# Kernel optimization log

Measured on AMD Instinct MI355X. Metric: run time of the kernel, lower is better.

Reference implementation:

```python
import jax, jax.numpy as jnp
import numpy as np

EPS = 1e-5

def _ln(x):
    # LayerNorm without affine (elementwise_affine=False when adaLN=True)
    m = jnp.mean(x, axis=-1, keepdims=True)
    v = jnp.mean((x - m) ** 2, axis=-1, keepdims=True)
    return (x - m) / jnp.sqrt(v + EPS)

def _ln_affine(x, g, b):
    return _ln(x) * g + b

def setup_inputs() -> dict:
    key = jax.random.key(0)
    B, L, D, H, P = 2, 1024, 1024, 16, 64
    FF = 4 * D
    ks = jax.random.split(key, 16)
    s = 0.02
    inp = {
        'x': jax.random.normal(ks[0], (B, L, D), jnp.float32),
        'z': jax.random.normal(ks[1], (B, L, L, P), jnp.float32),
        'trans': jax.random.normal(ks[2], (B, L, 3), jnp.float32),
        'mask': jnp.ones((B, L), jnp.bool_),
        'x_cond': jax.random.normal(ks[3], (B, L, D), jnp.float32),
        # adaLN modulation: SiLU -> Linear(D, 6D). (Randomly init'd; the torch
        # code zero-inits it, which would zero the whole block output.)
        'ada_W': jax.random.normal(ks[4], (D, 6 * D), jnp.float32) * s,
        'ada_b': jnp.zeros((6 * D,), jnp.float32),
        # attention projections (torch Linear weights stored as [in, out])
        'Wq': jax.random.normal(ks[5], (D, D), jnp.float32) * s,
        'bq': jnp.zeros((D,), jnp.float32),
        'Wk': jax.random.normal(ks[6], (D, D), jnp.float32) * s,
        'bk': jnp.zeros((D,), jnp.float32),
        'Wv': jax.random.normal(ks[7], (D, D), jnp.float32) * s,
        'bv': jnp.zeros((D,), jnp.float32),
        'Wo': jax.random.normal(ks[8], (D, D), jnp.float32) * s,
        'bo': jnp.zeros((D,), jnp.float32),
        # FeedForward: LayerNorm(D) (affine) -> Linear(D,FF) -> ReLU -> Linear(FF,D)
        'ln_g': jnp.ones((D,), jnp.float32),
        'ln_b': jnp.zeros((D,), jnp.float32),
        'W1': jax.random.normal(ks[9], (D, FF), jnp.float32) * s,
        'b1': jnp.zeros((FF,), jnp.float32),
        'W2': jax.random.normal(ks[10], (FF, D), jnp.float32) * s,
        'b2': jnp.zeros((D,), jnp.float32),
    }
    return inp

def _block(x, z, trans, mask, x_cond, ada_W, ada_b, Wq, bq, Wk, bk, Wv, bv,
           Wo, bo, ln_g, ln_b, W1, b1, W2, b2):
    B, L, D = x.shape
    H = 16
    dh = D // H
    # adaLN modulation from conditioning signal
    c = jax.nn.silu(x_cond) @ ada_W + ada_b
    (shift_mha, scale_mha, gate_mha,
     shift_mlp, scale_mlp, gate_mlp) = jnp.split(c, 6, axis=-1)
    # --- attention branch: norm -> modulate -> MHA -> gate -> residual ---
    h = _ln(x) * (1.0 + scale_mha) + shift_mha
    q = (h @ Wq + bq).reshape(B, L, H, dh)
    k = (h @ Wk + bk).reshape(B, L, H, dh)
    v = (h @ Wv + bv).reshape(B, L, H, dh)
    scores = jnp.einsum('blhd,bmhd->bhlm', q, k) / jnp.sqrt(jnp.float32(dh))
    neg = jnp.finfo(scores.dtype).min
    scores = jnp.where(mask[:, None, None, :], scores, neg)
    attn = jax.nn.softmax(scores, axis=-1)
    o = jnp.einsum('bhlm,bmhd->blhd', attn, v).reshape(B, L, D)
    mha_out = o @ Wo + bo
    x = x + mha_out * gate_mha
    # --- FFN branch: norm -> modulate -> FF(LN, Lin, ReLU, Lin) -> gate ---
    h = _ln(x) * (1.0 + scale_mlp) + shift_mlp
    h = _ln_affine(h, ln_g, ln_b)
    h = jax.nn.relu(h @ W1 + b1)
    ff_out = h @ W2 + b2
    x = x + ff_out * gate_mlp
    # pair_updates=False, frame_update=False: z and trans pass through
    return x, z, trans

def reference(x, z, trans, mask, x_cond, ada_W, ada_b, Wq, bq, Wk, bk, Wv, bv,
              Wo, bo, ln_g, ln_b, W1, b1, W2, b2):
    return _block(x, z, trans, mask, x_cond, ada_W, ada_b, Wq, bq, Wk, bk,
                  Wv, bv, Wo, bo, ln_g, ln_b, W1, b1, W2, b2)
```

## Files before the change

kernel.cpp:

```cpp
#include <hip/hip_runtime.h>
#include <hip/hip_bf16.h>


typedef __attribute__((ext_vector_type(8))) __bf16 bf16x8;
typedef __attribute__((ext_vector_type(4))) float f32x4;
typedef __attribute__((ext_vector_type(8))) unsigned short ushortx8;

#define DEVI static __device__ __forceinline__

DEVI unsigned short f2bf(float f) {
    __hip_bfloat16 h = __float2bfloat16(f);
    return __builtin_bit_cast(unsigned short, h);
}

DEVI void gload16(const void* g, void* l) {
    __builtin_amdgcn_global_load_lds(
        (const __attribute__((address_space(1))) void*)g,
        (__attribute__((address_space(3))) void*)l, 16, 0, 0);
}

DEVI void side_copy(const float4* __restrict__ src, float4* __restrict__ dst,
                    long long off, long long len, long long cb, long long ncb) {
    const long long nthr = ncb * 256;
    for (long long i = cb * 256 + threadIdx.x; i < len; i += nthr)
        dst[off + i] = src[off + i];
}

__global__ __launch_bounds__(256) void transpose_cast(
        const float* __restrict__ in, unsigned short* __restrict__ out,
        int K, int N) {
    __shared__ float tile[32][33];
    const int n0 = blockIdx.x * 32, k0 = blockIdx.y * 32;
    const int tx = threadIdx.x, ty = threadIdx.y;
#pragma unroll
    for (int i = 0; i < 4; ++i)
        tile[ty + 8 * i][tx] = in[(size_t)(k0 + ty + 8 * i) * N + n0 + tx];
    __syncthreads();
#pragma unroll
    for (int i = 0; i < 4; ++i)
        out[(size_t)(n0 + ty + 8 * i) * K + k0 + tx] = f2bf(tile[tx][ty + 8 * i]);
}

__global__ __launch_bounds__(256) void silu_cast(
        const float* __restrict__ x, unsigned short* __restrict__ o) {
    const int i = blockIdx.x * 256 + threadIdx.x;
    float4 v = ((const float4*)x)[i];
    ushort4 r;
    r.x = f2bf(v.x / (1.f + __expf(-v.x)));
    r.y = f2bf(v.y / (1.f + __expf(-v.y)));
    r.z = f2bf(v.z / (1.f + __expf(-v.z)));
    r.w = f2bf(v.w / (1.f + __expf(-v.w)));
    ((ushort4*)o)[i] = r;
}

__global__ void concat3(const float* __restrict__ a, const float* __restrict__ b,
                        const float* __restrict__ c, float* __restrict__ o, int D) {
    const int i = blockIdx.x * 256 + threadIdx.x;
    if (i < D) o[i] = a[i];
    else if (i < 2 * D) o[i] = b[i - D];
    else if (i < 3 * D) o[i] = c[i - 2 * D];
}

template <int MODE, int MT>
__global__ __launch_bounds__(256) void gemm_bt(
        const unsigned short* __restrict__ A, const unsigned short* __restrict__ Bt,
        const float* __restrict__ bias,
        float* __restrict__ outf, unsigned short* __restrict__ outb,
        const float* __restrict__ res, const float* __restrict__ gate, int gstride,
        int M, int N, int K,
        unsigned short* __restrict__ vt, int twoD, int H, int Lr,
        const float4* __restrict__ cp_src, float4* __restrict__ cp_dst,
        long long cp_off, long long cp_len, int gy) {
    if ((int)blockIdx.y >= gy) {
        const long long cb = (long long)(blockIdx.y - gy) * gridDim.x + blockIdx.x;
        const long long ncb = (long long)(gridDim.y - gy) * gridDim.x;
        side_copy(cp_src, cp_dst, cp_off, cp_len, cb, ncb);
        return;
    }
    __shared__ __align__(16) unsigned short lA[MT * 32 * 32];
    __shared__ __align__(16) unsigned short lB[128 * 32];
    const int tid = threadIdx.x;
    const int wave = tid >> 6, lane = tid & 63;
    const int fr = lane & 15, fg = lane >> 4;
    const int wr = wave >> 1, wc = wave & 1;
    const int m0 = blockIdx.y * (MT * 32), n0 = blockIdx.x * 128;

    f32x4 acc[MT][4];
#pragma unroll
    for (int i = 0; i < MT; ++i)
#pragma unroll
        for (int j = 0; j < 4; ++j) acc[i][j] = (f32x4){0.f, 0.f, 0.f, 0.f};

    for (int k0 = 0; k0 < K; k0 += 32) {
#pragma unroll
        for (int ch = 0; ch < 2; ++ch) {
            const int p = ch * 4096 + wave * 1024 + lane * 16;
            const int row = p >> 6, kb = p & 63;
            if (ch < MT / 2)
                gload16((const char*)A + ((size_t)(m0 + row) * K + k0) * 2 + kb, (char*)lA + p);
            gload16((const char*)Bt + ((size_t)(n0 + row) * K + k0) * 2 + kb, (char*)lB + p);
        }
        __syncthreads();
        bf16x8 af[MT], bfm[4];
#pragma unroll
        for (int t = 0; t < MT; ++t)
            af[t] = *(const bf16x8*)((const char*)lA + ((wr * (MT * 16) + t * 16 + fr) * 32 + fg * 8) * 2);
#pragma unroll
        for (int t = 0; t < 4; ++t)
            bfm[t] = *(const bf16x8*)((const char*)lB + ((wc * 64 + t * 16 + fr) * 32 + fg * 8) * 2);
#pragma unroll
        for (int mt = 0; mt < MT; ++mt)
#pragma unroll
            for (int nt = 0; nt < 4; ++nt)
                acc[mt][nt] = __builtin_amdgcn_mfma_f32_16x16x32_bf16(
                        af[mt], bfm[nt], acc[mt][nt], 0, 0, 0);
        __syncthreads();
    }
#pragma unroll
    for (int mt = 0; mt < MT; ++mt)
#pragma unroll
        for (int nt = 0; nt < 4; ++nt) {
            const int gcol = n0 + wc * 64 + nt * 16 + fr;
            const float bb = bias[gcol];
#pragma unroll
            for (int j = 0; j < 4; ++j) {
                const int grow = m0 + wr * (MT * 16) + mt * 16 + fg * 4 + j;
                const size_t idx = (size_t)grow * N + gcol;
                const float v = acc[mt][nt][j] + bb;
                if constexpr (MODE == 0) outf[idx] = v;
                else if constexpr (MODE == 1) outb[idx] = f2bf(v);
                else if constexpr (MODE == 2) outf[idx] = res[idx] + v * gate[(size_t)grow * gstride + gcol];
                else if constexpr (MODE == 3) outb[idx] = f2bf(fmaxf(v, 0.f));
                else {
                    const unsigned short bv16 = f2bf(v);
                    outb[idx] = bv16;
                    if (gcol >= twoD) {
                        const int d = gcol - twoD, hh = d >> 6, dd = d & 63;
                        const int bb2 = grow >= Lr ? 1 : 0, l = grow - bb2 * Lr;
                        vt[((size_t)(bb2 * H + hh) * 64 + dd) * Lr + l] = bv16;
                    }
                }
            }
        }
}

__global__ __launch_bounds__(256) void ln_mod(
        const float* __restrict__ x, const float* __restrict__ c,
        unsigned short* __restrict__ h, int D, int cs) {
    const int row = blockIdx.x, tid = threadIdx.x;
    const int lane = tid & 63, wave = tid >> 6;
    const float4 xv = ((const float4*)(x + (size_t)row * D))[tid];
    float s = xv.x + xv.y + xv.z + xv.w;
    float ss = xv.x * xv.x + xv.y * xv.y + xv.z * xv.z + xv.w * xv.w;
#pragma unroll
    for (int o = 1; o < 64; o <<= 1) { s += __shfl_xor(s, o); ss += __shfl_xor(ss, o); }
    __shared__ float red[8];
    if (lane == 0) { red[wave] = s; red[4 + wave] = ss; }
    __syncthreads();
    s = red[0] + red[1] + red[2] + red[3];
    ss = red[4] + red[5] + red[6] + red[7];
    const float mean = s / D;
    const float rstd = rsqrtf(ss / D - mean * mean + 1e-5f);
    const float* crow = c + (size_t)row * cs;
    const float4 sh = ((const float4*)(crow))[tid];
    const float4 sc = ((const float4*)(crow + D))[tid];
    ushort4 r;
    r.x = f2bf((xv.x - mean) * rstd * (1.f + sc.x) + sh.x);
    r.y = f2bf((xv.y - mean) * rstd * (1.f + sc.y) + sh.y);
    r.z = f2bf((xv.z - mean) * rstd * (1.f + sc.z) + sh.z);
    r.w = f2bf((xv.w - mean) * rstd * (1.f + sc.w) + sh.w);
    ((ushort4*)(h + (size_t)row * D))[tid] = r;
}

__global__ __launch_bounds__(256) void ln2_mod(
        const float* __restrict__ x2, const float* __restrict__ c,
        const float* __restrict__ g, const float* __restrict__ bb,
        unsigned short* __restrict__ h, int D, int cs) {
    const int row = blockIdx.x, tid = threadIdx.x;
    const int lane = tid & 63, wave = tid >> 6;
    const float4 xv = ((const float4*)(x2 + (size_t)row * D))[tid];
    float s = xv.x + xv.y + xv.z + xv.w;
    float ss = xv.x * xv.x + xv.y * xv.y + xv.z * xv.z + xv.w * xv.w;
#pragma unroll
    for (int o = 1; o < 64; o <<= 1) { s += __shfl_xor(s, o); ss += __shfl_xor(ss, o); }
    __shared__ float red[16];
    if (lane == 0) { red[wave] = s; red[4 + wave] = ss; }
    __syncthreads();
    s = red[0] + red[1] + red[2] + red[3];
    ss = red[4] + red[5] + red[6] + red[7];
    const float mean = s / D;
    const float rstd = rsqrtf(ss / D - mean * mean + 1e-5f);
    const float* crow = c + (size_t)row * cs;
    const float4 sh = ((const float4*)(crow + 3 * D))[tid];
    const float4 sc = ((const float4*)(crow + 4 * D))[tid];
    float t[4];
    t[0] = (xv.x - mean) * rstd * (1.f + sc.x) + sh.x;
    t[1] = (xv.y - mean) * rstd * (1.f + sc.y) + sh.y;
    t[2] = (xv.z - mean) * rstd * (1.f + sc.z) + sh.z;
    t[3] = (xv.w - mean) * rstd * (1.f + sc.w) + sh.w;
    float s2 = t[0] + t[1] + t[2] + t[3];
    float ss2 = t[0] * t[0] + t[1] * t[1] + t[2] * t[2] + t[3] * t[3];
#pragma unroll
    for (int o = 1; o < 64; o <<= 1) { s2 += __shfl_xor(s2, o); ss2 += __shfl_xor(ss2, o); }
    if (lane == 0) { red[8 + wave] = s2; red[12 + wave] = ss2; }
    __syncthreads();
    s2 = red[8] + red[9] + red[10] + red[11];
    ss2 = red[12] + red[13] + red[14] + red[15];
    const float mean2 = s2 / D;
    const float rstd2 = rsqrtf(ss2 / D - mean2 * mean2 + 1e-5f);
    const float4 gv = ((const float4*)g)[tid];
    const float4 bv = ((const float4*)bb)[tid];
    ushort4 r;
    r.x = f2bf((t[0] - mean2) * rstd2 * gv.x + bv.x);
    r.y = f2bf((t[1] - mean2) * rstd2 * gv.y + bv.y);
    r.z = f2bf((t[2] - mean2) * rstd2 * gv.z + bv.z);
    r.w = f2bf((t[3] - mean2) * rstd2 * gv.w + bv.w);
    ((ushort4*)(h + (size_t)row * D))[tid] = r;
}

__global__ __launch_bounds__(256) void attn_fwd(
        const unsigned short* __restrict__ qkv, const unsigned short* __restrict__ vt,
        unsigned short* __restrict__ o,
        int L, int D, int B,
        const float4* __restrict__ cp_src, float4* __restrict__ cp_dst,
        long long cp_off, long long cp_len) {
    if ((int)blockIdx.z >= B) {
        const long long cb = (long long)(blockIdx.z - B) * gridDim.x * gridDim.y
                           + (long long)blockIdx.y * gridDim.x + blockIdx.x;
        const long long ncb = (long long)(gridDim.z - B) * gridDim.x * gridDim.y;
        side_copy(cp_src, cp_dst, cp_off, cp_len, cb, ncb);
        return;
    }
    const int q0 = blockIdx.x * 64, hh = blockIdx.y, b = blockIdx.z;
    const int H = gridDim.y;
    const int tid = threadIdx.x, wave = tid >> 6, lane = tid & 63;
    const int fr = lane & 15, fg = lane >> 4;
    const size_t rs = 3 * (size_t)D;
    const unsigned short* vtb = vt + (size_t)(b * H + hh) * 64 * L;
    __shared__ __align__(16) unsigned short lK[64 * 72];
    __shared__ __align__(16) unsigned short lVT[64 * 72];
    __shared__ __align__(16) unsigned short lP[4 * 16 * 72];

    bf16x8 aq[2];
    {
        const size_t qr = (size_t)(b * L + q0 + wave * 16 + fr);
#pragma unroll
        for (int kk = 0; kk < 2; ++kk)
            aq[kk] = *(const bf16x8*)(qkv + qr * rs + hh * 64 + kk * 32 + fg * 8);
    }
    f32x4 oacc[4];
#pragma unroll
    for (int i = 0; i < 4; ++i) oacc[i] = (f32x4){0.f, 0.f, 0.f, 0.f};
    float m_run[4] = {-1e30f, -1e30f, -1e30f, -1e30f};
    float l_run[4] = {0.f, 0.f, 0.f, 0.f};

    for (int n0 = 0; n0 < L; n0 += 64) {
        __syncthreads();
#pragma unroll
        for (int it = 0; it < 2; ++it) {
            const int idx = it * 256 + tid, r = idx >> 3, cc = idx & 7;
            const unsigned short* src = qkv + (size_t)(b * L + n0 + r) * rs + D + hh * 64 + cc * 8;
            *(ushortx8*)(&lK[r * 72 + cc * 8]) = *(const ushortx8*)src;
        }
#pragma unroll
        for (int it = 0; it < 2; ++it) {
            const int idx = it * 256 + tid, r = idx >> 3, cc = idx & 7;
            *(ushortx8*)(&lVT[r * 72 + cc * 8]) =
                *(const ushortx8*)(vtb + (size_t)r * L + n0 + cc * 8);
        }
        __syncthreads();
        f32x4 sfr[4];
#pragma unroll
        for (int nt = 0; nt < 4; ++nt) {
            const bf16x8 bk0 = *(const bf16x8*)((const char*)lK + ((nt * 16 + fr) * 72 + fg * 8) * 2);
            const bf16x8 bk1 = *(const bf16x8*)((const char*)lK + ((nt * 16 + fr) * 72 + 32 + fg * 8) * 2);
            f32x4 t = (f32x4){0.f, 0.f, 0.f, 0.f};
            t = __builtin_amdgcn_mfma_f32_16x16x32_bf16(aq[0], bk0, t, 0, 0, 0);
            t = __builtin_amdgcn_mfma_f32_16x16x32_bf16(aq[1], bk1, t, 0, 0, 0);
#pragma unroll
            for (int j = 0; j < 4; ++j) t[j] *= 0.125f;
            sfr[nt] = t;
        }
        float tm[4], prs[4], alpha[4];
#pragma unroll
        for (int j = 0; j < 4; ++j) {
            float v = fmaxf(fmaxf(sfr[0][j], sfr[1][j]), fmaxf(sfr[2][j], sfr[3][j]));
#pragma unroll
            for (int off = 1; off < 16; off <<= 1) v = fmaxf(v, __shfl_xor(v, off));
            tm[j] = v;
        }
#pragma unroll
        for (int j = 0; j < 4; ++j) {
            const float mn = fmaxf(m_run[j], tm[j]);
            alpha[j] = __expf(m_run[j] - mn);
            m_run[j] = mn;
            prs[j] = 0.f;
        }
#pragma unroll
        for (int nt = 0; nt < 4; ++nt)
#pragma unroll
            for (int j = 0; j < 4; ++j) {
                const float p = __expf(sfr[nt][j] - m_run[j]);
                sfr[nt][j] = p;
                prs[j] += p;
            }
#pragma unroll
        for (int j = 0; j < 4; ++j) {
#pragma unroll
            for (int off = 1; off < 16; off <<= 1) prs[j] += __shfl_xor(prs[j], off);
            l_run[j] = l_run[j] * alpha[j] + prs[j];
        }
#pragma unroll
        for (int dt = 0; dt < 4; ++dt)
#pragma unroll
            for (int j = 0; j < 4; ++j) oacc[dt][j] *= alpha[j];
        unsigned short* pw = &lP[wave * 16 * 72];
#pragma unroll
        for (int nt = 0; nt < 4; ++nt)
#pragma unroll
            for (int j = 0; j < 4; ++j)
                pw[(fg * 4 + j) * 72 + nt * 16 + fr] = f2bf(sfr[nt][j]);
        const bf16x8 ap0 = *(const bf16x8*)((const char*)pw + (fr * 72 + fg * 8) * 2);
        const bf16x8 ap1 = *(const bf16x8*)((const char*)pw + (fr * 72 + 32 + fg * 8) * 2);
#pragma unroll
        for (int dt = 0; dt < 4; ++dt) {
            const bf16x8 bv0 = *(const bf16x8*)((const char*)lVT + ((dt * 16 + fr) * 72 + fg * 8) * 2);
            const bf16x8 bv1 = *(const bf16x8*)((const char*)lVT + ((dt * 16 + fr) * 72 + 32 + fg * 8) * 2);
            oacc[dt] = __builtin_amdgcn_mfma_f32_16x16x32_bf16(ap0, bv0, oacc[dt], 0, 0, 0);
            oacc[dt] = __builtin_amdgcn_mfma_f32_16x16x32_bf16(ap1, bv1, oacc[dt], 0, 0, 0);
        }
    }
    float inv[4];
#pragma unroll
    for (int j = 0; j < 4; ++j) inv[j] = 1.f / l_run[j];
#pragma unroll
    for (int dt = 0; dt < 4; ++dt)
#pragma unroll
        for (int j = 0; j < 4; ++j) {
            const int orow = b * L + q0 + wave * 16 + fg * 4 + j;
            o[(size_t)orow * D + hh * 64 + dt * 16 + fr] = f2bf(oacc[dt][j] * inv[j]);
        }
}

extern "C" void kernel_launch(void* const* d_in, const int* in_sizes, int n_in,
                              void* d_out, int out_size, void* d_ws, size_t ws_size,
                              hipStream_t stream) {
    (void)n_in; (void)out_size;
    const float* x      = (const float*)d_in[0];
    const float* z      = (const float*)d_in[1];
    const float* trans  = (const float*)d_in[2];
    const float* x_cond = (const float*)d_in[4];
    const float* ada_W  = (const float*)d_in[5];
    const float* ada_b  = (const float*)d_in[6];
    const float* Wq = (const float*)d_in[7];  const float* bq = (const float*)d_in[8];
    const float* Wk = (const float*)d_in[9];  const float* bk = (const float*)d_in[10];
    const float* Wv = (const float*)d_in[11]; const float* bv = (const float*)d_in[12];
    const float* Wo = (const float*)d_in[13]; const float* bo = (const float*)d_in[14];
    const float* ln_g = (const float*)d_in[15]; const float* ln_b = (const float*)d_in[16];
    const float* W1 = (const float*)d_in[17]; const float* b1 = (const float*)d_in[18];
    const float* W2 = (const float*)d_in[19]; const float* b2 = (const float*)d_in[20];

    const int D  = in_sizes[6] / 6;
    const int FF = in_sizes[18];
    const int M  = in_sizes[0] / D;
    const int B  = 2, L = M / B, H = 16;
    const size_t zN = (size_t)in_sizes[1], tN = (size_t)in_sizes[2];

    float* out_x = (float*)d_out;
    float* out_z = out_x + (size_t)M * D;
    float* out_t = out_z + zN;

    size_t off = 0;
    auto alloc = [&](size_t bytes) { size_t o = off; off += (bytes + 255) & ~(size_t)255; return o; };
    const size_t o_adaWt = alloc((size_t)6 * D * D * 2);
    const size_t o_Wqkvt = alloc((size_t)3 * D * D * 2);
    const size_t o_Wot   = alloc((size_t)D * D * 2);
    const size_t o_W1t   = alloc((size_t)FF * D * 2);
    const size_t o_W2t   = alloc((size_t)D * FF * 2);
    const size_t o_bqkv  = alloc((size_t)3 * D * 4);
    const size_t o_xcb   = alloc((size_t)M * D * 2);
    const size_t o_c     = alloc((size_t)M * 6 * D * 4);
    const size_t o_hb    = alloc((size_t)M * D * 2);
    const size_t o_qkv   = alloc((size_t)M * 3 * D * 2);
    const size_t o_vt    = alloc((size_t)M * D * 2);
    const size_t o_ob    = alloc((size_t)M * D * 2);
    const size_t o_x2    = alloc((size_t)M * D * 4);
    const size_t o_h2b   = alloc((size_t)M * D * 2);
    const size_t o_f1    = alloc((size_t)M * FF * 2);
    const size_t need = off;
    const bool have_ws = (ws_size >= need);
    char* base = have_ws ? (char*)d_ws : (char*)out_z;

    unsigned short* adaWt = (unsigned short*)(base + o_adaWt);
    unsigned short* Wqkvt = (unsigned short*)(base + o_Wqkvt);
    unsigned short* Wot   = (unsigned short*)(base + o_Wot);
    unsigned short* W1t   = (unsigned short*)(base + o_W1t);
    unsigned short* W2t   = (unsigned short*)(base + o_W2t);
    float*          bqkv  = (float*)(base + o_bqkv);
    unsigned short* xcb   = (unsigned short*)(base + o_xcb);
    float*          cbuf  = (float*)(base + o_c);
    unsigned short* hb    = (unsigned short*)(base + o_hb);
    unsigned short* qkvb  = (unsigned short*)(base + o_qkv);
    unsigned short* vtb   = (unsigned short*)(base + o_vt);
    unsigned short* ob    = (unsigned short*)(base + o_ob);
    float*          x2    = (float*)(base + o_x2);
    unsigned short* h2b   = (unsigned short*)(base + o_h2b);
    unsigned short* f1b   = (unsigned short*)(base + o_f1);

    const float4* zs = (const float4*)z;
    float4* zd = (float4*)out_z;
    const long long zN4 = (long long)(zN / 4);
    long long c0 = 0, c1 = 0, c2 = 0, c3 = 0, c4 = 0, c5 = 0;
    int e0 = 0, e1 = 0, e2 = 0, e3 = 0, e4 = 0, e5 = 0;
    if (have_ws) {
        c0 = zN4 / 4;  c1 = zN4 / 8;  c2 = zN4 / 4;  c3 = zN4 / 16;  c4 = zN4 / 4;
        c5 = zN4 - (c0 + c1 + c2 + c3 + c4);
        e0 = 8; e1 = 16; e2 = 1; e3 = 16; e4 = 12; e5 = 24;
    }
    const long long s0 = 0, s1 = s0 + c0, s2 = s1 + c1, s3 = s2 + c2, s4 = s3 + c3, s5 = s4 + c4;

    const dim3 tb(32, 8);
    transpose_cast<<<dim3(6 * D / 32, D / 32), tb, 0, stream>>>(ada_W, adaWt, D, 6 * D);
    transpose_cast<<<dim3(D / 32, D / 32), tb, 0, stream>>>(Wq, Wqkvt, D, D);
    transpose_cast<<<dim3(D / 32, D / 32), tb, 0, stream>>>(Wk, Wqkvt + (size_t)D * D, D, D);
    transpose_cast<<<dim3(D / 32, D / 32), tb, 0, stream>>>(Wv, Wqkvt + (size_t)2 * D * D, D, D);
    transpose_cast<<<dim3(D / 32, D / 32), tb, 0, stream>>>(Wo, Wot, D, D);
    transpose_cast<<<dim3(FF / 32, D / 32), tb, 0, stream>>>(W1, W1t, D, FF);
    transpose_cast<<<dim3(D / 32, FF / 32), tb, 0, stream>>>(W2, W2t, FF, D);
    concat3<<<(3 * D + 255) / 256, 256, 0, stream>>>(bq, bk, bv, bqkv, D);
    silu_cast<<<M * D / 1024, 256, 0, stream>>>(x_cond, xcb);

    const int gy128 = M / 128, gy64 = M / 64;
    gemm_bt<0, 4><<<dim3(6 * D / 128, gy128 + e0), 256, 0, stream>>>(
            xcb, adaWt, ada_b, cbuf, nullptr, nullptr, nullptr, 0, M, 6 * D, D,
            nullptr, 0, 0, 0, zs, zd, s0, c0, gy128);
    ln_mod<<<M, 256, 0, stream>>>(x, cbuf, hb, D, 6 * D);
    gemm_bt<4, 4><<<dim3(3 * D / 128, gy128 + e1), 256, 0, stream>>>(
            hb, Wqkvt, bqkv, nullptr, qkvb, nullptr, nullptr, 0, M, 3 * D, D,
            vtb, 2 * D, H, L, zs, zd, s1, c1, gy128);
    attn_fwd<<<dim3(L / 64, H, B + e2), 256, 0, stream>>>(qkvb, vtb, ob, L, D, B,
            zs, zd, s2, c2);
    gemm_bt<2, 2><<<dim3(D / 128, gy64 + e3), 256, 0, stream>>>(
            ob, Wot, bo, x2, nullptr, x, cbuf + 2 * D, 6 * D, M, D, D,
            nullptr, 0, 0, 0, zs, zd, s3, c3, gy64);
    ln2_mod<<<M, 256, 0, stream>>>(x2, cbuf, ln_g, ln_b, h2b, D, 6 * D);
    gemm_bt<3, 4><<<dim3(FF / 128, gy128 + e4), 256, 0, stream>>>(
            h2b, W1t, b1, nullptr, f1b, nullptr, nullptr, 0, M, FF, D,
            nullptr, 0, 0, 0, zs, zd, s4, c4, gy128);
    gemm_bt<2, 2><<<dim3(D / 128, gy64 + e5), 256, 0, stream>>>(
            f1b, W2t, b2, out_x, nullptr, x2, cbuf + 5 * D, 6 * D, M, D, FF,
            nullptr, 0, 0, 0, zs, zd, s5, c5, gy64);

    if (!have_ws) {
        hipMemcpyAsync(out_z, z, zN * 4, hipMemcpyDeviceToDevice, stream);
    } else if (zN % 4) {
        const size_t done = (size_t)zN4 * 4;
        hipMemcpyAsync(out_z + done, z + done, (zN - done) * 4,
                       hipMemcpyDeviceToDevice, stream);
    }
    hipMemcpyAsync(out_t, trans, tN * 4, hipMemcpyDeviceToDevice, stream);
}
```

Baseline: 1.268 ms.

## Move entire z pass-through copy into attention kernel side blocks

Drops the z copy work that was spread across all six GEMM and attention launches. The whole z tensor is now copied by extra blocks appended to the attention kernel's grid (6 extra z-slices). This removes copy-branch overhead and extra blocks from the GEMMs. The cost is that attention overlap must now hide the full 512MB copy, and the copy is done by fewer blocks. It also drops the tail memcpy for a z length not divisible by 4, which is only safe for the fixed shape.

```diff
diff --git a/kernel.cpp b/kernel.cpp
--- a/kernel.cpp
+++ b/kernel.cpp
@@ -20,10 +20,10 @@
 }
 
 DEVI void side_copy(const float4* __restrict__ src, float4* __restrict__ dst,
-                    long long off, long long len, long long cb, long long ncb) {
+                    long long len, long long cb, long long ncb) {
     const long long nthr = ncb * 256;
     for (long long i = cb * 256 + threadIdx.x; i < len; i += nthr)
-        dst[off + i] = src[off + i];
+        dst[i] = src[i];
 }
 
 __global__ __launch_bounds__(256) void transpose_cast(
@@ -68,15 +68,7 @@
         float* __restrict__ outf, unsigned short* __restrict__ outb,
         const float* __restrict__ res, const float* __restrict__ gate, int gstride,
         int M, int N, int K,
-        unsigned short* __restrict__ vt, int twoD, int H, int Lr,
-        const float4* __restrict__ cp_src, float4* __restrict__ cp_dst,
-        long long cp_off, long long cp_len, int gy) {
-    if ((int)blockIdx.y >= gy) {
-        const long long cb = (long long)(blockIdx.y - gy) * gridDim.x + blockIdx.x;
-        const long long ncb = (long long)(gridDim.y - gy) * gridDim.x;
-        side_copy(cp_src, cp_dst, cp_off, cp_len, cb, ncb);
-        return;
-    }
+        unsigned short* __restrict__ vt, int twoD, int H, int Lr) {
     __shared__ __align__(16) unsigned short lA[MT * 32 * 32];
     __shared__ __align__(16) unsigned short lB[128 * 32];
     const int tid = threadIdx.x;
@@ -223,12 +215,12 @@
         unsigned short* __restrict__ o,
         int L, int D, int B,
         const float4* __restrict__ cp_src, float4* __restrict__ cp_dst,
-        long long cp_off, long long cp_len) {
+        long long cp_len) {
     if ((int)blockIdx.z >= B) {
         const long long cb = (long long)(blockIdx.z - B) * gridDim.x * gridDim.y
                            + (long long)blockIdx.y * gridDim.x + blockIdx.x;
         const long long ncb = (long long)(gridDim.z - B) * gridDim.x * gridDim.y;
-        side_copy(cp_src, cp_dst, cp_off, cp_len, cb, ncb);
+        side_copy(cp_src, cp_dst, cp_len, cb, ncb);
         return;
     }
     const int q0 = blockIdx.x * 64, hh = blockIdx.y, b = blockIdx.z;
@@ -410,14 +402,8 @@
     const float4* zs = (const float4*)z;
     float4* zd = (float4*)out_z;
     const long long zN4 = (long long)(zN / 4);
-    long long c0 = 0, c1 = 0, c2 = 0, c3 = 0, c4 = 0, c5 = 0;
-    int e0 = 0, e1 = 0, e2 = 0, e3 = 0, e4 = 0, e5 = 0;
-    if (have_ws) {
-        c0 = zN4 / 4;  c1 = zN4 / 8;  c2 = zN4 / 4;  c3 = zN4 / 16;  c4 = zN4 / 4;
-        c5 = zN4 - (c0 + c1 + c2 + c3 + c4);
-        e0 = 8; e1 = 16; e2 = 1; e3 = 16; e4 = 12; e5 = 24;
-    }
-    const long long s0 = 0, s1 = s0 + c0, s2 = s1 + c1, s3 = s2 + c2, s4 = s3 + c3, s5 = s4 + c4;
+    const int ECOPY = have_ws ? 6 : 0;
+    const long long cplen = have_ws ? zN4 : 0;
 
     const dim3 tb(32, 8);
     transpose_cast<<<dim3(6 * D / 32, D / 32), tb, 0, stream>>>(ada_W, adaWt, D, 6 * D);
@@ -431,32 +417,28 @@
     silu_cast<<<M * D / 1024, 256, 0, stream>>>(x_cond, xcb);
 
     const int gy128 = M / 128, gy64 = M / 64;
-    gemm_bt<0, 4><<<dim3(6 * D / 128, gy128 + e0), 256, 0, stream>>>(
+    gemm_bt<0, 4><<<dim3(6 * D / 128, gy128), 256, 0, stream>>>(
             xcb, adaWt, ada_b, cbuf, nullptr, nullptr, nullptr, 0, M, 6 * D, D,
-            nullptr, 0, 0, 0, zs, zd, s0, c0, gy128);
+            nullptr, 0, 0, 0);
     ln_mod<<<M, 256, 0, stream>>>(x, cbuf, hb, D, 6 * D);
-    gemm_bt<4, 4><<<dim3(3 * D / 128, gy128 + e1), 256, 0, stream>>>(
+    gemm_bt<4, 4><<<dim3(3 * D / 128, gy128), 256, 0, stream>>>(
             hb, Wqkvt, bqkv, nullptr, qkvb, nullptr, nullptr, 0, M, 3 * D, D,
-            vtb, 2 * D, H, L, zs, zd, s1, c1, gy128);
-    attn_fwd<<<dim3(L / 64, H, B + e2), 256, 0, stream>>>(qkvb, vtb, ob, L, D, B,
-            zs, zd, s2, c2);
-    gemm_bt<2, 2><<<dim3(D / 128, gy64 + e3), 256, 0, stream>>>(
+            vtb, 2 * D, H, L);
+    attn_fwd<<<dim3(L / 64, H, B + ECOPY), 256, 0, stream>>>(qkvb, vtb, ob, L, D, B,
+            zs, zd, cplen);
+    gemm_bt<2, 2><<<dim3(D / 128, gy64), 256, 0, stream>>>(
             ob, Wot, bo, x2, nullptr, x, cbuf + 2 * D, 6 * D, M, D, D,
-            nullptr, 0, 0, 0, zs, zd, s3, c3, gy64);
+            nullptr, 0, 0, 0);
     ln2_mod<<<M, 256, 0, stream>>>(x2, cbuf, ln_g, ln_b, h2b, D, 6 * D);
-    gemm_bt<3, 4><<<dim3(FF / 128, gy128 + e4), 256, 0, stream>>>(
+    gemm_bt<3, 4><<<dim3(FF / 128, gy128), 256, 0, stream>>>(
             h2b, W1t, b1, nullptr, f1b, nullptr, nullptr, 0, M, FF, D,
-            nullptr, 0, 0, 0, zs, zd, s4, c4, gy128);
-    gemm_bt<2, 2><<<dim3(D / 128, gy64 + e5), 256, 0, stream>>>(
+            nullptr, 0, 0, 0);
+    gemm_bt<2, 2><<<dim3(D / 128, gy64), 256, 0, stream>>>(
             f1b, W2t, b2, out_x, nullptr, x2, cbuf + 5 * D, 6 * D, M, D, FF,
-            nullptr, 0, 0, 0, zs, zd, s5, c5, gy64);
+            nullptr, 0, 0, 0);
 
     if (!have_ws) {
         hipMemcpyAsync(out_z, z, zN * 4, hipMemcpyDeviceToDevice, stream);
-    } else if (zN % 4) {
-        const size_t done = (size_t)zN4 * 4;
-        hipMemcpyAsync(out_z + done, z + done, (zN - done) * 4,
-                       hipMemcpyDeviceToDevice, stream);
     }
     hipMemcpyAsync(out_t, trans, tN * 4, hipMemcpyDeviceToDevice, stream);
 }
```

Result: faster. 1.213 ms (-4.3%).
